# Performance work log

Hardware: AMD Instinct MI355X
Metric: run time of the kernel (lower is better)

Reference implementation:

```python
import jax, jax.numpy as jnp
import numpy as np
import math

B, N, D_MODEL, H, D_HEAD = 2, 2048, 1024, 16, 64
EPS = 1e-6

def setup_inputs() -> dict:
    key = jax.random.key(0)
    ks = jax.random.split(key, 6)
    s = 1.0 / math.sqrt(D_MODEL)
    return {
        "X": jax.random.normal(ks[0], (B, N, D_MODEL), dtype=jnp.float32),
        "Wq": jax.random.normal(ks[1], (D_MODEL, H * D_HEAD), dtype=jnp.float32) * s,
        "Wk": jax.random.normal(ks[2], (D_MODEL, H * D_HEAD), dtype=jnp.float32) * s,
        "Wv": jax.random.normal(ks[3], (D_MODEL, H * D_HEAD), dtype=jnp.float32) * s,
        "Wo": jax.random.normal(ks[4], (H * D_HEAD, D_MODEL), dtype=jnp.float32) * s,
        "bo": jnp.zeros((D_MODEL,), dtype=jnp.float32),
    }

def reference(X, Wq, Wk, Wv, Wo, bo):
    b, n, _ = X.shape
    # project and split heads -> [b, h, n, d_head]
    def heads(Y):
        return Y.reshape(b, n, H, D_HEAD).transpose(0, 2, 1, 3)
    Q = heads(X @ Wq)
    K = heads(X @ Wk)
    V = heads(X @ Wv)
    # per-head L2 normalization of Q and K
    Q = Q / (jnp.linalg.norm(Q, axis=-1, keepdims=True) + EPS)
    K = K / (jnp.linalg.norm(K, axis=-1, keepdims=True) + EPS)
    # scores [b, h, n, n]
    A = jnp.einsum("bhqd,bhkd->bhqk", Q, K) / math.sqrt(D_HEAD)
    causal = jnp.triu(jnp.ones((n, n), dtype=bool), k=1)
    A = jnp.where(causal, -jnp.inf, A)
    A = jax.nn.softmax(A, axis=-1)
    V_hat = jnp.einsum("bhqk,bhkd->bhqd", A, V)
    V_hat = V_hat.transpose(0, 2, 1, 3).reshape(b, n, H * D_HEAD)
    return V_hat @ Wo + bo
```

## Files before the change

kernel.cpp:

```cpp
#include <hip/hip_runtime.h>
#include <hip/hip_bf16.h>
#include <math.h>

#define BATCH 2
#define NSEQ  2048
#define DM    1024
#define NH    16
#define DH    64
#define EPS_N 1e-6f

typedef unsigned short u16;
typedef __attribute__((ext_vector_type(8))) short short8;
typedef __attribute__((ext_vector_type(8))) unsigned short u16x8;
typedef __attribute__((ext_vector_type(4))) unsigned short u16x4;
typedef __attribute__((ext_vector_type(4))) float f32x4;

__device__ __forceinline__ u16 f2bf(float x) {
  __hip_bfloat16 h = __float2bfloat16(x);
  return *reinterpret_cast<u16*>(&h);
}

__device__ __forceinline__ void gl_lds16(const u16* g, u16* lds_base) {
  __builtin_amdgcn_global_load_lds(
      (__attribute__((address_space(1))) void*)g,
      (__attribute__((address_space(3))) void*)lds_base, 16, 0, 0);
}

__global__ __launch_bounds__(256) void prep(
    const float* __restrict__ X,
    const float* __restrict__ w0, const float* __restrict__ w1,
    const float* __restrict__ w2, const float* __restrict__ w3,
    u16* __restrict__ Xb, u16* __restrict__ WT) {
  const int id = blockIdx.x, tid = threadIdx.x;
  if (id >= 1024) {
    size_t base = ((size_t)(id - 1024) * 256 + tid) * 8;
    float4 f0 = *(const float4*)&X[base];
    float4 f1 = *(const float4*)&X[base + 4];
    u16x8 v;
    v[0] = f2bf(f0.x); v[1] = f2bf(f0.y); v[2] = f2bf(f0.z); v[3] = f2bf(f0.w);
    v[4] = f2bf(f1.x); v[5] = f2bf(f1.y); v[6] = f2bf(f1.z); v[7] = f2bf(f1.w);
    *(u16x8*)&Xb[base] = v;
    return;
  }
  const int z = id >> 8, xy = id & 255, bx = xy & 15, by = xy >> 4;
  const float* in = (z == 0) ? w0 : (z == 1) ? w1 : (z == 2) ? w2 : w3;
  u16* o = WT + (size_t)z * DM * DM;
  __shared__ u16 T[64][65];
  const int n0 = bx * 64, k0 = by * 64;
  #pragma unroll
  for (int i = 0; i < 4; i++) {
    int c = tid + 256 * i, row = c >> 4, col4 = c & 15;
    float4 f = *(const float4*)&in[(size_t)(k0 + row) * DM + n0 + col4 * 4];
    T[row][col4 * 4 + 0] = f2bf(f.x);
    T[row][col4 * 4 + 1] = f2bf(f.y);
    T[row][col4 * 4 + 2] = f2bf(f.z);
    T[row][col4 * 4 + 3] = f2bf(f.w);
  }
  __syncthreads();
  #pragma unroll
  for (int i = 0; i < 2; i++) {
    int c = tid + 256 * i, row = c >> 3, col8 = c & 7;
    u16x8 v;
    #pragma unroll
    for (int e = 0; e < 8; e++) v[e] = T[col8 * 8 + e][row];
    *(u16x8*)&o[(size_t)(n0 + row) * DM + k0 + col8 * 8] = v;
  }
}

#define GEMM128_MAINLOOP(Aptr, Btptr)                                          \
  __shared__ u16 As[128 * 64];                                                 \
  __shared__ u16 Bs[128 * 64];                                                 \
  const int tid = threadIdx.x, w = tid >> 6, lane = tid & 63;                  \
  const int ml = lane & 15, quad = lane >> 4;                                  \
  const int m0 = blockIdx.y * 128, n0 = blockIdx.x * 128;                      \
  const int wm = w & 1, wn = w >> 1;                                           \
  const int srow = lane >> 3;                      \
  const int scol = ((lane & 7) ^ srow) * 8;         \
  f32x4 acc[4][4];                                                             \
  _Pragma("unroll") for (int mi = 0; mi < 4; mi++)                             \
    _Pragma("unroll") for (int ni = 0; ni < 4; ni++)                           \
      _Pragma("unroll") for (int e = 0; e < 4; e++) acc[mi][ni][e] = 0.f;      \
  for (int k0 = 0; k0 < DM; k0 += 64) {                                        \
    __syncthreads();                                                           \
    _Pragma("unroll") for (int L = 0; L < 4; L++) {                            \
      int I = w * 4 + L;                                                       \
      gl_lds16(Aptr  + (size_t)(m0 + I * 8 + srow) * DM + k0 + scol,           \
               As + I * 512);                                                  \
      gl_lds16(Btptr + (size_t)(n0 + I * 8 + srow) * DM + k0 + scol,           \
               Bs + I * 512);                                                  \
    }                                                                          \
    __syncthreads();                                                           \
    _Pragma("unroll") for (int kk = 0; kk < 64; kk += 32) {                    \
      const int kc = kk >> 3;                          \
      short8 am[4], bn[4];                                                     \
      _Pragma("unroll") for (int i = 0; i < 4; i++) {                          \
        int ra = wm * 64 + i * 16 + ml;                                        \
        int rb = wn * 64 + i * 16 + ml;                                        \
        am[i] = *(const short8*)&As[ra * 64 + (((quad + kc) ^ (ra & 7)) * 8)]; \
        bn[i] = *(const short8*)&Bs[rb * 64 + (((quad + kc) ^ (rb & 7)) * 8)]; \
      }                                                                        \
      _Pragma("unroll") for (int mi = 0; mi < 4; mi++)                         \
        _Pragma("unroll") for (int ni = 0; ni < 4; ni++)                       \
          acc[mi][ni] = __builtin_amdgcn_mfma_f32_16x16x32_bf16(               \
              am[mi], bn[ni], acc[mi][ni], 0, 0, 0);                           \
    }                                                                          \
  }

__global__ __launch_bounds__(256) void gemm_qkv128(
    const u16* __restrict__ Xb, const u16* __restrict__ WT,
    u16* __restrict__ Qo, u16* __restrict__ Ko, u16* __restrict__ Vt) {
  const u16* Bt = WT + (size_t)blockIdx.z * DM * DM;
  GEMM128_MAINLOOP(Xb, Bt)
  const int z = blockIdx.z;
  if (z < 2) {
    u16* OutQK = (z == 0) ? Qo : Ko;
    const float qsc = (z == 0) ? 0.125f : 1.0f;
    const int h = (n0 >> 6) + wn;
    #pragma unroll
    for (int mi = 0; mi < 4; mi++) {
      int mrow0 = m0 + wm * 64 + mi * 16 + quad * 4;
      int b = mrow0 >> 11, tok0 = mrow0 & (NSEQ - 1);
      #pragma unroll
      for (int r = 0; r < 4; r++) {
        float ss = 0.f;
        #pragma unroll
        for (int ni = 0; ni < 4; ni++) ss += acc[mi][ni][r] * acc[mi][ni][r];
        ss += __shfl_xor(ss, 1, 64);
        ss += __shfl_xor(ss, 2, 64);
        ss += __shfl_xor(ss, 4, 64);
        ss += __shfl_xor(ss, 8, 64);
        float sc = qsc / (sqrtf(ss) + EPS_N);
        #pragma unroll
        for (int ni = 0; ni < 4; ni++)
          OutQK[((size_t)(b * NH + h) * NSEQ + tok0 + r) * DH + ni * 16 + ml] =
              f2bf(acc[mi][ni][r] * sc);
      }
    }
  } else {
    #pragma unroll
    for (int mi = 0; mi < 4; mi++) {
      int mrow0 = m0 + wm * 64 + mi * 16 + quad * 4;
      int b = mrow0 >> 11, tok0 = mrow0 & (NSEQ - 1);
      #pragma unroll
      for (int ni = 0; ni < 4; ni++) {
        int n = n0 + wn * 64 + ni * 16 + ml;
        int h = n >> 6, d = n & 63;
        u16x4 pk;
        #pragma unroll
        for (int r = 0; r < 4; r++) pk[r] = f2bf(acc[mi][ni][r]);
        *(u16x4*)&Vt[((size_t)(b * NH + h) * DH + d) * NSEQ + tok0] = pk;
      }
    }
  }
}

__global__ __launch_bounds__(256) void gemm_proj128(
    const u16* __restrict__ A, const u16* __restrict__ BtW,
    const float* __restrict__ bias, float* __restrict__ out) {
  GEMM128_MAINLOOP(A, BtW)
  #pragma unroll
  for (int ni = 0; ni < 4; ni++) {
    int n = n0 + wn * 64 + ni * 16 + ml;
    float bz = bias[n];
    #pragma unroll
    for (int mi = 0; mi < 4; mi++) {
      int mrow0 = m0 + wm * 64 + mi * 16 + quad * 4;
      #pragma unroll
      for (int r = 0; r < 4; r++)
        out[(size_t)(mrow0 + r) * DM + n] = acc[mi][ni][r] + bz;
    }
  }
}

__global__ __launch_bounds__(64) void flash_attn(
    const u16* __restrict__ Qb, const u16* __restrict__ Kb,
    const u16* __restrict__ Vt, u16* __restrict__ vhat) {
  const int lane = threadIdx.x;
  const int ml = lane & 15, quad = lane >> 4;
  const int bh = blockIdx.x;
  const int bb = bh >> 4, hb = bh & 15;
  const int qblk = 63 - (int)blockIdx.y;
  const int q0 = qblk * 32;
  const int nsteps = qblk + 1;
  const u16* Qh = Qb + (size_t)bh * NSEQ * DH;
  const u16* Kh = Kb + (size_t)bh * NSEQ * DH;
  const u16* Vth = Vt + (size_t)bh * DH * NSEQ;

  __shared__ u16 Ps[32][40];

  short8 aq[2][2];
  #pragma unroll
  for (int m = 0; m < 2; m++)
    #pragma unroll
    for (int c = 0; c < 2; c++)
      aq[m][c] = *(const short8*)
          &Qh[(size_t)(q0 + m * 16 + ml) * DH + c * 32 + quad * 8];

  f32x4 oacc[2][4];
  #pragma unroll
  for (int m = 0; m < 2; m++)
    #pragma unroll
    for (int n = 0; n < 4; n++)
      #pragma unroll
      for (int e = 0; e < 4; e++) oacc[m][n][e] = 0.f;
  float l_[2][4] = {{0.f, 0.f, 0.f, 0.f}, {0.f, 0.f, 0.f, 0.f}};

  short8 kf[2][2];
  #pragma unroll
  for (int n = 0; n < 2; n++)
    #pragma unroll
    for (int c = 0; c < 2; c++)
      kf[n][c] = *(const short8*)
          &Kh[(size_t)(n * 16 + ml) * DH + c * 32 + quad * 8];

  for (int s = 0; s < nsteps; s++) {
    const int j0 = s * 32;
    short8 vf[4];
    #pragma unroll
    for (int n = 0; n < 4; n++)
      vf[n] = *(const short8*)&Vth[(size_t)(n * 16 + ml) * NSEQ + j0 + quad * 8];

    f32x4 sacc[2][2];
    #pragma unroll
    for (int m = 0; m < 2; m++)
      #pragma unroll
      for (int n = 0; n < 2; n++) {
        #pragma unroll
        for (int e = 0; e < 4; e++) sacc[m][n][e] = 0.f;
        #pragma unroll
        for (int c = 0; c < 2; c++)
          sacc[m][n] = __builtin_amdgcn_mfma_f32_16x16x32_bf16(
              aq[m][c], kf[n][c], sacc[m][n], 0, 0, 0);
      }

    const int j0n = (j0 + 32 < NSEQ) ? (j0 + 32) : (NSEQ - 32);
    #pragma unroll
    for (int n = 0; n < 2; n++)
      #pragma unroll
      for (int c = 0; c < 2; c++)
        kf[n][c] = *(const short8*)
            &Kh[(size_t)(j0n + n * 16 + ml) * DH + c * 32 + quad * 8];

    const bool lastt = (s == nsteps - 1);
    #pragma unroll
    for (int m = 0; m < 2; m++)
      #pragma unroll
      for (int n = 0; n < 2; n++) {
        int j = j0 + n * 16 + ml;
        #pragma unroll
        for (int r = 0; r < 4; r++) {
          int q = q0 + m * 16 + quad * 4 + r;
          float e = __expf(sacc[m][n][r]);
          e = (lastt && j > q) ? 0.f : e;
          l_[m][r] += e;
          Ps[m * 16 + quad * 4 + r][n * 16 + ml] = f2bf(e);
        }
      }

    #pragma unroll
    for (int m = 0; m < 2; m++) {
      short8 ap = *(const short8*)&Ps[m * 16 + ml][quad * 8];
      #pragma unroll
      for (int n = 0; n < 4; n++)
        oacc[m][n] = __builtin_amdgcn_mfma_f32_16x16x32_bf16(
            ap, vf[n], oacc[m][n], 0, 0, 0);
    }
  }

  #pragma unroll
  for (int m = 0; m < 2; m++)
    #pragma unroll
    for (int r = 0; r < 4; r++) {
      float lv = l_[m][r];
      lv += __shfl_xor(lv, 1, 64);
      lv += __shfl_xor(lv, 2, 64);
      lv += __shfl_xor(lv, 4, 64);
      lv += __shfl_xor(lv, 8, 64);
      float inv = 1.f / lv;
      int q = q0 + m * 16 + quad * 4 + r;
      #pragma unroll
      for (int n = 0; n < 4; n++)
        vhat[((size_t)(bb * NSEQ + q)) * DM + hb * DH + n * 16 + ml] =
            f2bf(oacc[m][n][r] * inv);
    }
}

extern "C" void kernel_launch(void* const* d_in, const int* in_sizes, int n_in,
                              void* d_out, int out_size, void* d_ws, size_t ws_size,
                              hipStream_t stream) {
  const float* X  = (const float*)d_in[0];
  const float* Wq = (const float*)d_in[1];
  const float* Wk = (const float*)d_in[2];
  const float* Wv = (const float*)d_in[3];
  const float* Wo = (const float*)d_in[4];
  const float* bo = (const float*)d_in[5];
  float* out = (float*)d_out;

  const size_t NE = (size_t)BATCH * NSEQ * DM;
  u16* Qb   = (u16*)d_ws;
  u16* Kb   = Qb + NE;
  u16* Vt   = Kb + NE;
  u16* XbVh = Vt + NE;
  u16* WT   = XbVh + NE;

  prep        <<<dim3(3072),      256, 0, stream>>>(X, Wq, Wk, Wv, Wo, XbVh, WT);
  gemm_qkv128 <<<dim3(8, 32, 3),  256, 0, stream>>>(XbVh, WT, Qb, Kb, Vt);
  flash_attn  <<<dim3(32, 64),     64, 0, stream>>>(Qb, Kb, Vt, XbVh);
  gemm_proj128<<<dim3(8, 32, 1),  256, 0, stream>>>(XbVh, WT + 3 * (size_t)DM * DM,
                                                    bo, out);
}
```

Measured before the change: 224.3 us.

## Split attention KV loop across two waves and fold log2e into Q scale

The flash attention kernel now runs two waves per block, each handling alternating 32-key tiles of the causal range. The partial outputs and row sums are merged through shared memory before the final normalization and store. Separately, the Q scale now includes log2(e), so the kernel can call the hardware exp2 instead of __expf. This halves the serial loop length per wave, which targets the latency-bound single-wave loop, at the cost of an LDS reduction, a barrier and more shared memory per block.

```diff
diff --git a/kernel.cpp b/kernel.cpp
--- a/kernel.cpp
+++ b/kernel.cpp
@@ -114,7 +114,7 @@
   const int z = blockIdx.z;
   if (z < 2) {
     u16* OutQK = (z == 0) ? Qo : Ko;
-    const float qsc = (z == 0) ? 0.125f : 1.0f;
+    const float qsc = (z == 0) ? 0.125f * 1.44269504f : 1.0f;
     const int h = (n0 >> 6) + wn;
     #pragma unroll
     for (int mi = 0; mi < 4; mi++) {
@@ -172,21 +172,22 @@
   }
 }
 
-__global__ __launch_bounds__(64) void flash_attn(
+__global__ __launch_bounds__(128) void flash_attn(
     const u16* __restrict__ Qb, const u16* __restrict__ Kb,
     const u16* __restrict__ Vt, u16* __restrict__ vhat) {
-  const int lane = threadIdx.x;
+  const int tid = threadIdx.x, w = tid >> 6, lane = tid & 63;
   const int ml = lane & 15, quad = lane >> 4;
   const int bh = blockIdx.x;
   const int bb = bh >> 4, hb = bh & 15;
   const int qblk = 63 - (int)blockIdx.y;
   const int q0 = qblk * 32;
-  const int nsteps = qblk + 1;
   const u16* Qh = Qb + (size_t)bh * NSEQ * DH;
   const u16* Kh = Kb + (size_t)bh * NSEQ * DH;
   const u16* Vth = Vt + (size_t)bh * DH * NSEQ;
 
-  __shared__ u16 Ps[32][40];
+  __shared__ u16 Ps[2][32][40];
+  __shared__ float Ob[2][4][64][4];
+  __shared__ float Lb[2][64][4];
 
   short8 aq[2][2];
   #pragma unroll
@@ -211,10 +212,10 @@
     #pragma unroll
     for (int c = 0; c < 2; c++)
       kf[n][c] = *(const short8*)
-          &Kh[(size_t)(n * 16 + ml) * DH + c * 32 + quad * 8];
-
-  for (int s = 0; s < nsteps; s++) {
-    const int j0 = s * 32;
+          &Kh[(size_t)(w * 32 + n * 16 + ml) * DH + c * 32 + quad * 8];
+
+  for (int t = w; t <= qblk; t += 2) {
+    const int j0 = t * 32;
     short8 vf[4];
     #pragma unroll
     for (int n = 0; n < 4; n++)
@@ -233,7 +234,7 @@
               aq[m][c], kf[n][c], sacc[m][n], 0, 0, 0);
       }
 
-    const int j0n = (j0 + 32 < NSEQ) ? (j0 + 32) : (NSEQ - 32);
+    const int j0n = (t + 2 <= qblk) ? (t + 2) * 32 : j0;
     #pragma unroll
     for (int n = 0; n < 2; n++)
       #pragma unroll
@@ -241,7 +242,7 @@
         kf[n][c] = *(const short8*)
             &Kh[(size_t)(j0n + n * 16 + ml) * DH + c * 32 + quad * 8];
 
-    const bool lastt = (s == nsteps - 1);
+    const bool lastt = (t == qblk);
     #pragma unroll
     for (int m = 0; m < 2; m++)
       #pragma unroll
@@ -250,16 +251,16 @@
         #pragma unroll
         for (int r = 0; r < 4; r++) {
           int q = q0 + m * 16 + quad * 4 + r;
-          float e = __expf(sacc[m][n][r]);
+          float e = __builtin_amdgcn_exp2f(sacc[m][n][r]);
           e = (lastt && j > q) ? 0.f : e;
           l_[m][r] += e;
-          Ps[m * 16 + quad * 4 + r][n * 16 + ml] = f2bf(e);
+          Ps[w][m * 16 + quad * 4 + r][n * 16 + ml] = f2bf(e);
         }
       }
 
     #pragma unroll
     for (int m = 0; m < 2; m++) {
-      short8 ap = *(const short8*)&Ps[m * 16 + ml][quad * 8];
+      short8 ap = *(const short8*)&Ps[w][m * 16 + ml][quad * 8];
       #pragma unroll
       for (int n = 0; n < 4; n++)
         oacc[m][n] = __builtin_amdgcn_mfma_f32_16x16x32_bf16(
@@ -267,22 +268,47 @@
     }
   }
 
-  #pragma unroll
-  for (int m = 0; m < 2; m++)
-    #pragma unroll
-    for (int r = 0; r < 4; r++) {
-      float lv = l_[m][r];
-      lv += __shfl_xor(lv, 1, 64);
-      lv += __shfl_xor(lv, 2, 64);
-      lv += __shfl_xor(lv, 4, 64);
-      lv += __shfl_xor(lv, 8, 64);
-      float inv = 1.f / lv;
-      int q = q0 + m * 16 + quad * 4 + r;
+  if (w == 1) {
+    #pragma unroll
+    for (int m = 0; m < 2; m++) {
       #pragma unroll
       for (int n = 0; n < 4; n++)
-        vhat[((size_t)(bb * NSEQ + q)) * DM + hb * DH + n * 16 + ml] =
-            f2bf(oacc[m][n][r] * inv);
-    }
+        *(f32x4*)&Ob[m][n][lane][0] = oacc[m][n];
+      f32x4 lv = {l_[m][0], l_[m][1], l_[m][2], l_[m][3]};
+      *(f32x4*)&Lb[m][lane][0] = lv;
+    }
+  }
+  __syncthreads();
+  if (w == 0) {
+    #pragma unroll
+    for (int m = 0; m < 2; m++) {
+      f32x4 lv = *(const f32x4*)&Lb[m][lane][0];
+      #pragma unroll
+      for (int r = 0; r < 4; r++) l_[m][r] += lv[r];
+      #pragma unroll
+      for (int n = 0; n < 4; n++) {
+        f32x4 o2 = *(const f32x4*)&Ob[m][n][lane][0];
+        #pragma unroll
+        for (int e = 0; e < 4; e++) oacc[m][n][e] += o2[e];
+      }
+    }
+    #pragma unroll
+    for (int m = 0; m < 2; m++)
+      #pragma unroll
+      for (int r = 0; r < 4; r++) {
+        float lv = l_[m][r];
+        lv += __shfl_xor(lv, 1, 64);
+        lv += __shfl_xor(lv, 2, 64);
+        lv += __shfl_xor(lv, 4, 64);
+        lv += __shfl_xor(lv, 8, 64);
+        float inv = 1.f / lv;
+        int q = q0 + m * 16 + quad * 4 + r;
+        #pragma unroll
+        for (int n = 0; n < 4; n++)
+          vhat[((size_t)(bb * NSEQ + q)) * DM + hb * DH + n * 16 + ml] =
+              f2bf(oacc[m][n][r] * inv);
+      }
+  }
 }
 
 extern "C" void kernel_launch(void* const* d_in, const int* in_sizes, int n_in,
@@ -305,7 +331,7 @@
 
   prep        <<<dim3(3072),      256, 0, stream>>>(X, Wq, Wk, Wv, Wo, XbVh, WT);
   gemm_qkv128 <<<dim3(8, 32, 3),  256, 0, stream>>>(XbVh, WT, Qb, Kb, Vt);
-  flash_attn  <<<dim3(32, 64),     64, 0, stream>>>(Qb, Kb, Vt, XbVh);
+  flash_attn  <<<dim3(32, 64),    128, 0, stream>>>(Qb, Kb, Vt, XbVh);
   gemm_proj128<<<dim3(8, 32, 1),  256, 0, stream>>>(XbVh, WT + 3 * (size_t)DM * DM,
                                                     bo, out);
 }
```

Measured after the change: 224.2 us. About the same (-0.0%).

## Restructure flash attention into 4-wave blocks sharing LDS-staged K/V tiles

Applied to the files above, without the earlier changes.

The attention kernel moves from one-wave blocks over 32 queries to 256-thread blocks covering 128 queries. K and V tiles of 64 keys are staged in swizzled LDS through global_load_lds, so all four waves reuse one copy instead of each reading global memory. Each block processes a pair of mirrored query blocks (long and short causal rows) to balance work, and exp is replaced by exp2 with log2(e) folded into the Q scale. This adds two __syncthreads per tile and drops the register prefetch of K, so global loads are no longer overlapped with compute.

```diff
diff --git a/kernel.cpp b/kernel.cpp
--- a/kernel.cpp
+++ b/kernel.cpp
@@ -114,7 +114,7 @@
   const int z = blockIdx.z;
   if (z < 2) {
     u16* OutQK = (z == 0) ? Qo : Ko;
-    const float qsc = (z == 0) ? 0.125f : 1.0f;
+    const float qsc = (z == 0) ? 0.125f * 1.44269504f : 1.0f;
     const int h = (n0 >> 6) + wn;
     #pragma unroll
     for (int mi = 0; mi < 4; mi++) {
@@ -172,117 +172,128 @@
   }
 }
 
-__global__ __launch_bounds__(64) void flash_attn(
+__global__ __launch_bounds__(256) void flash_attn(
     const u16* __restrict__ Qb, const u16* __restrict__ Kb,
     const u16* __restrict__ Vt, u16* __restrict__ vhat) {
-  const int lane = threadIdx.x;
+  const int tid = threadIdx.x, w = tid >> 6, lane = tid & 63;
   const int ml = lane & 15, quad = lane >> 4;
   const int bh = blockIdx.x;
   const int bb = bh >> 4, hb = bh & 15;
-  const int qblk = 63 - (int)blockIdx.y;
-  const int q0 = qblk * 32;
-  const int nsteps = qblk + 1;
   const u16* Qh = Qb + (size_t)bh * NSEQ * DH;
   const u16* Kh = Kb + (size_t)bh * NSEQ * DH;
   const u16* Vth = Vt + (size_t)bh * DH * NSEQ;
 
-  __shared__ u16 Ps[32][40];
-
-  short8 aq[2][2];
-  #pragma unroll
-  for (int m = 0; m < 2; m++)
-    #pragma unroll
-    for (int c = 0; c < 2; c++)
-      aq[m][c] = *(const short8*)
-          &Qh[(size_t)(q0 + m * 16 + ml) * DH + c * 32 + quad * 8];
-
-  f32x4 oacc[2][4];
-  #pragma unroll
-  for (int m = 0; m < 2; m++)
-    #pragma unroll
-    for (int n = 0; n < 4; n++)
-      #pragma unroll
-      for (int e = 0; e < 4; e++) oacc[m][n][e] = 0.f;
-  float l_[2][4] = {{0.f, 0.f, 0.f, 0.f}, {0.f, 0.f, 0.f, 0.f}};
-
-  short8 kf[2][2];
-  #pragma unroll
-  for (int n = 0; n < 2; n++)
-    #pragma unroll
-    for (int c = 0; c < 2; c++)
-      kf[n][c] = *(const short8*)
-          &Kh[(size_t)(n * 16 + ml) * DH + c * 32 + quad * 8];
-
-  for (int s = 0; s < nsteps; s++) {
-    const int j0 = s * 32;
-    short8 vf[4];
-    #pragma unroll
-    for (int n = 0; n < 4; n++)
-      vf[n] = *(const short8*)&Vth[(size_t)(n * 16 + ml) * NSEQ + j0 + quad * 8];
-
-    f32x4 sacc[2][2];
+  __shared__ u16 Ks [64 * 64];
+  __shared__ u16 VsT[64 * 64];
+  __shared__ u16 Ps [4][32][76];
+
+  const int srow = lane >> 3;
+  const int scol = ((lane & 7) ^ srow) * 8;
+
+  for (int ph = 0; ph < 2; ph++) {
+    const int qblk = ph ? (int)blockIdx.y : (15 - (int)blockIdx.y);
+    const int q0 = qblk * 128;
+    const int ntiles = 2 * (qblk + 1);
+
+    short8 aq[2][2];
     #pragma unroll
     for (int m = 0; m < 2; m++)
       #pragma unroll
-      for (int n = 0; n < 2; n++) {
-        #pragma unroll
-        for (int e = 0; e < 4; e++) sacc[m][n][e] = 0.f;
-        #pragma unroll
-        for (int c = 0; c < 2; c++)
-          sacc[m][n] = __builtin_amdgcn_mfma_f32_16x16x32_bf16(
-              aq[m][c], kf[n][c], sacc[m][n], 0, 0, 0);
-      }
-
-    const int j0n = (j0 + 32 < NSEQ) ? (j0 + 32) : (NSEQ - 32);
-    #pragma unroll
-    for (int n = 0; n < 2; n++)
-      #pragma unroll
       for (int c = 0; c < 2; c++)
-        kf[n][c] = *(const short8*)
-            &Kh[(size_t)(j0n + n * 16 + ml) * DH + c * 32 + quad * 8];
-
-    const bool lastt = (s == nsteps - 1);
+        aq[m][c] = *(const short8*)
+            &Qh[(size_t)(q0 + w * 32 + m * 16 + ml) * DH + c * 32 + quad * 8];
+
+    f32x4 oacc[2][4];
     #pragma unroll
     for (int m = 0; m < 2; m++)
       #pragma unroll
-      for (int n = 0; n < 2; n++) {
-        int j = j0 + n * 16 + ml;
-        #pragma unroll
-        for (int r = 0; r < 4; r++) {
-          int q = q0 + m * 16 + quad * 4 + r;
-          float e = __expf(sacc[m][n][r]);
-          e = (lastt && j > q) ? 0.f : e;
-          l_[m][r] += e;
-          Ps[m * 16 + quad * 4 + r][n * 16 + ml] = f2bf(e);
+      for (int n = 0; n < 4; n++)
+        #pragma unroll
+        for (int e = 0; e < 4; e++) oacc[m][n][e] = 0.f;
+    float l_[2][4] = {{0.f, 0.f, 0.f, 0.f}, {0.f, 0.f, 0.f, 0.f}};
+
+    for (int t = 0; t < ntiles; t++) {
+      const int j0 = t * 64;
+      __syncthreads();
+      #pragma unroll
+      for (int i2 = 0; i2 < 2; i2++) {
+        int i = w + 4 * i2;
+        gl_lds16(Kh  + (size_t)(j0 + i * 8 + srow) * DH + scol, Ks  + i * 512);
+        gl_lds16(Vth + (size_t)(i * 8 + srow) * NSEQ + j0 + scol, VsT + i * 512);
+      }
+      __syncthreads();
+
+      f32x4 sacc[2][4];
+      #pragma unroll
+      for (int m = 0; m < 2; m++)
+        #pragma unroll
+        for (int n = 0; n < 4; n++)
+          #pragma unroll
+          for (int e = 0; e < 4; e++) sacc[m][n][e] = 0.f;
+      #pragma unroll
+      for (int c = 0; c < 2; c++)
+        #pragma unroll
+        for (int n = 0; n < 4; n++) {
+          int rk = n * 16 + ml;
+          short8 kf = *(const short8*)
+              &Ks[rk * 64 + (((c * 4 + quad) ^ (rk & 7)) * 8)];
+          #pragma unroll
+          for (int m = 0; m < 2; m++)
+            sacc[m][n] = __builtin_amdgcn_mfma_f32_16x16x32_bf16(
+                aq[m][c], kf, sacc[m][n], 0, 0, 0);
         }
-      }
-
-    #pragma unroll
-    for (int m = 0; m < 2; m++) {
-      short8 ap = *(const short8*)&Ps[m * 16 + ml][quad * 8];
-      #pragma unroll
-      for (int n = 0; n < 4; n++)
-        oacc[m][n] = __builtin_amdgcn_mfma_f32_16x16x32_bf16(
-            ap, vf[n], oacc[m][n], 0, 0, 0);
+
+      #pragma unroll
+      for (int m = 0; m < 2; m++)
+        #pragma unroll
+        for (int n = 0; n < 4; n++) {
+          int j = j0 + n * 16 + ml;
+          #pragma unroll
+          for (int r = 0; r < 4; r++) {
+            int q = q0 + w * 32 + m * 16 + quad * 4 + r;
+            float e = __builtin_amdgcn_exp2f(sacc[m][n][r]);
+            e = (j > q) ? 0.f : e;
+            l_[m][r] += e;
+            Ps[w][m * 16 + quad * 4 + r][n * 16 + ml] = f2bf(e);
+          }
+        }
+
+      #pragma unroll
+      for (int c = 0; c < 2; c++) {
+        short8 ap[2];
+        #pragma unroll
+        for (int m = 0; m < 2; m++)
+          ap[m] = *(const short8*)&Ps[w][m * 16 + ml][c * 32 + quad * 8];
+        #pragma unroll
+        for (int n = 0; n < 4; n++) {
+          int rv = n * 16 + ml;
+          short8 bv = *(const short8*)
+              &VsT[rv * 64 + (((c * 4 + quad) ^ (rv & 7)) * 8)];
+          #pragma unroll
+          for (int m = 0; m < 2; m++)
+            oacc[m][n] = __builtin_amdgcn_mfma_f32_16x16x32_bf16(
+                ap[m], bv, oacc[m][n], 0, 0, 0);
+        }
+      }
     }
-  }
-
-  #pragma unroll
-  for (int m = 0; m < 2; m++)
-    #pragma unroll
-    for (int r = 0; r < 4; r++) {
-      float lv = l_[m][r];
-      lv += __shfl_xor(lv, 1, 64);
-      lv += __shfl_xor(lv, 2, 64);
-      lv += __shfl_xor(lv, 4, 64);
-      lv += __shfl_xor(lv, 8, 64);
-      float inv = 1.f / lv;
-      int q = q0 + m * 16 + quad * 4 + r;
-      #pragma unroll
-      for (int n = 0; n < 4; n++)
-        vhat[((size_t)(bb * NSEQ + q)) * DM + hb * DH + n * 16 + ml] =
-            f2bf(oacc[m][n][r] * inv);
-    }
+
+    #pragma unroll
+    for (int m = 0; m < 2; m++)
+      #pragma unroll
+      for (int r = 0; r < 4; r++) {
+        float lv = l_[m][r];
+        lv += __shfl_xor(lv, 1, 64);
+        lv += __shfl_xor(lv, 2, 64);
+        lv += __shfl_xor(lv, 4, 64);
+        lv += __shfl_xor(lv, 8, 64);
+        float inv = 1.f / lv;
+        int q = q0 + w * 32 + m * 16 + quad * 4 + r;
+        #pragma unroll
+        for (int n = 0; n < 4; n++)
+          vhat[((size_t)(bb * NSEQ + q)) * DM + hb * DH + n * 16 + ml] =
+              f2bf(oacc[m][n][r] * inv);
+      }
+  }
 }
 
 extern "C" void kernel_launch(void* const* d_in, const int* in_sizes, int n_in,
@@ -305,7 +316,7 @@
 
   prep        <<<dim3(3072),      256, 0, stream>>>(X, Wq, Wk, Wv, Wo, XbVh, WT);
   gemm_qkv128 <<<dim3(8, 32, 3),  256, 0, stream>>>(XbVh, WT, Qb, Kb, Vt);
-  flash_attn  <<<dim3(32, 64),     64, 0, stream>>>(Qb, Kb, Vt, XbVh);
+  flash_attn  <<<dim3(32, 8),     256, 0, stream>>>(Qb, Kb, Vt, XbVh);
   gemm_proj128<<<dim3(8, 32, 1),  256, 0, stream>>>(XbVh, WT + 3 * (size_t)DM * DM,
                                                     bo, out);
 }
```

New measurement: 214.8 us. 4.2% less time.
